# Kernel tuning notes

Hardware: AMD Instinct MI355X
Metric: run time of the kernel (lower is better)

Reference implementation:

```python
import jax, jax.numpy as jnp
import numpy as np

# Baked genome DAG structure (static per-instance in the original module)
N_IN = 256
LAYER_SIZES = [256, 256, 256, 256, 64]  # 4 hidden layers + output layer
N_OUT = LAYER_SIZES[-1]
N_EVAL = sum(LAYER_SIZES)  # 1088 eval nodes (node_evals)
DEG = 32                   # incoming links per eval node
BATCH = 8192


def setup_inputs() -> dict:
    key = jax.random.key(0)
    kx, kw, kb, kr = jax.random.split(key, 4)
    x = jax.random.normal(kx, (BATCH, N_IN), dtype=jnp.float32)
    # connection weights, node bias, node response (learned genome params)
    w = jax.random.normal(kw, (N_EVAL, DEG), dtype=jnp.float32) * 0.5
    bias = jax.random.normal(kb, (N_EVAL,), dtype=jnp.float32) * 0.1
    response = 1.0 + jax.random.normal(kr, (N_EVAL,), dtype=jnp.float32) * 0.1
    # per-layer source indices: each eval node connects to DEG earlier nodes
    src_rows = []
    offset = N_IN  # number of nodes topologically before current layer
    for li, sz in enumerate(LAYER_SIZES):
        ks = jax.random.fold_in(key, 100 + li)
        src_rows.append(jax.random.randint(ks, (sz, DEG), 0, offset, dtype=jnp.int32))
        offset += sz
    src_idx = jnp.concatenate(src_rows, axis=0)  # [N_EVAL, DEG]
    return {"x": x, "w": w, "bias": bias, "response": response, "src_idx": src_idx}


def reference(x, w, bias, response, src_idx):
    # values: [B, n_nodes_so_far]; starts as the input node values
    values = x
    row = 0
    for sz in LAYER_SIZES:  # small fixed structural loop (topological layers)
        s = src_idx[row:row + sz]                       # [sz, DEG]
        gathered = values[:, s]                         # [B, sz, DEG]
        agg = jnp.einsum('bsd,sd->bs', gathered, w[row:row + sz])  # sum aggregation
        out = jax.nn.relu(bias[row:row + sz] + response[row:row + sz] * agg)
        values = jnp.concatenate([values, out], axis=1)
        row += sz
    return values[:, -N_OUT:]  # [B, N_OUT]
```

## Files before the change

### kernel.cpp

```cpp
#include <hip/hip_runtime.h>

#define N_IN   256
#define N_EVAL 1088
#define TOTALW 1344
#define DEG    32

typedef __attribute__((ext_vector_type(8))) short short8;
typedef __attribute__((ext_vector_type(4))) float f32x4;
typedef unsigned short u16;
typedef unsigned int   u32;

__device__ __forceinline__ u32 pk2(float lo, float hi) {
    u32 ul = __float_as_uint(lo);
    u32 uh = __float_as_uint(hi);
    ul = (ul + 0x7fffu + ((ul >> 16) & 1u)) >> 16;
    uh = (uh + 0x7fffu + ((uh >> 16) & 1u)) & 0xffff0000u;
    return ul | uh;
}
__device__ __forceinline__ u16 bf1(float v) {
    u32 u = __float_as_uint(v);
    return (u16)((u + 0x7fffu + ((u >> 16) & 1u)) >> 16);
}

__global__ __launch_bounds__(256) void build_dense32(
    const int* __restrict__ src, const float* __restrict__ w,
    u32* __restrict__ B32)
{
    const int t = blockIdx.x * 256 + threadIdx.x;
    const int tile = t >> 8;
    const int q    = t & 255;
    const int lane = q >> 2;
    const int e2   = q & 3;
    int li, ts;
    if      (tile < 128)  { li = 0; ts = 0;    }
    else if (tile < 384)  { li = 1; ts = 128;  }
    else if (tile < 768)  { li = 2; ts = 384;  }
    else if (tile < 1280) { li = 3; ts = 768;  }
    else                  { li = 4; ts = 1280; }
    const int tloc = tile - ts;
    int kt, nt;
    if (li < 4) { kt = tloc >> 4; nt = tloc & 15; }
    else        { kt = tloc >> 2; nt = tloc & 3;  }
    const int ln = lane & 15, g = lane >> 4;
    const int gn = li * 256 + nt * 16 + ln;
    const int k0 = kt * 32 + g * 8 + e2 * 2;

    int c[DEG]; float ow[DEG];
    const int4*   s4 = (const int4*)(src + (size_t)gn * DEG);
    const float4* w4 = (const float4*)(w   + (size_t)gn * DEG);
    #pragma unroll
    for (int k = 0; k < 8; ++k) {
        int4 ci = s4[k]; float4 wf = w4[k];
        c[4*k+0]=ci.x; c[4*k+1]=ci.y; c[4*k+2]=ci.z; c[4*k+3]=ci.w;
        ow[4*k+0]=wf.x; ow[4*k+1]=wf.y; ow[4*k+2]=wf.z; ow[4*k+3]=wf.w;
    }
    float s0 = 0.f, s1 = 0.f;
    #pragma unroll
    for (int d = 0; d < DEG; ++d) {
        s0 += (c[d] == k0    ) ? ow[d] : 0.f;
        s1 += (c[d] == k0 + 1) ? ow[d] : 0.f;
    }
    B32[t] = pk2(s0, s1);
}

#define TILE_B 32
#define LDSCOLS 1280
#define RSTRIDE (LDSCOLS * 2)

#define MFMA(a, b, c) __builtin_amdgcn_mfma_f32_16x16x32_bf16(a, b, c, 0, 0, 0)

__global__ __launch_bounds__(512) void neat_mfma(
    const float* __restrict__ x, const u16* __restrict__ Bbuf,
    const float* __restrict__ bias, const float* __restrict__ resp,
    float* __restrict__ out)
{
    __shared__ uint4 ldsq[(TILE_B * RSTRIDE) / 16];
    __shared__ f32x4 pbuf[4 * 64 * 2];
    char* lds = (char*)ldsq;
    const int tid  = threadIdx.x;
    const int bid  = blockIdx.x;
    const int b0   = bid * TILE_B;
    const int lane = tid & 63;
    const int wvid = tid >> 6;

    const short8* Bf = (const short8*)Bbuf;
    short8 rp0[8], rp1[8];
    {
        const int rot0 = bid & 7;
        const short8* bp0 = Bf + wvid * 64 + lane;
        const short8* bp1 = Bf + (wvid + 8) * 64 + lane;
        #pragma unroll
        for (int j = 0; j < 8; ++j) {
            int ph = j + rot0; if (ph >= 8) ph -= 8;
            rp0[j] = bp0[ph * 1024];
            rp1[j] = bp1[ph * 1024];
        }
    }

    #pragma unroll
    for (int i = 0; i < 4; ++i) {
        int f4 = tid + i * 512;
        int row = f4 >> 6;
        int c4  = f4 & 63;
        float4 xv = ((const float4*)(x + (size_t)(b0 + row) * N_IN))[c4];
        u32 p0 = pk2(xv.x, xv.y), p1 = pk2(xv.z, xv.w);
        int byte = row * RSTRIDE + ((c4 * 8) ^ ((row & 7) << 4));
        *(u32*)(lds + byte)     = p0;
        *(u32*)(lds + byte + 4) = p1;
    }
    __syncthreads();

    const int r0  = lane & 15;
    const int g16 = (lane >> 4) << 4;
    const int sw  = (r0 & 7) << 4;
    const int ab0 = r0 * RSTRIDE;
    const int ab1 = (r0 + 16) * RSTRIDE;

    int cbase = N_IN;
    #pragma unroll
    for (int li = 0; li < 5; ++li) {
        const int ktn = (N_IN + li * 256) >> 5;
        const int loff8[5] = {0, 8192, 24576, 49152, 81920};
        const int lo8 = loff8[li];
        const int nbase = cbase - N_IN;

        if (li < 4) {
            const int STEP = 16 * 64;
            const int rot  = bid % ktn;
            const int nt0 = wvid, nt1 = wvid + 8;
            const short8* bp0 = Bf + lo8 + nt0 * 64 + lane;
            const short8* bp1 = Bf + lo8 + nt1 * 64 + lane;
            const int gr0 = nbase + nt0 * 16 + r0;
            const int gr1 = nbase + nt1 * 16 + r0;
            const float bb0 = bias[gr0], rr0 = resp[gr0];
            const float bb1 = bias[gr1], rr1 = resp[gr1];

            f32x4 acc00 = {0,0,0,0}, acc01 = {0,0,0,0};
            f32x4 acc10 = {0,0,0,0}, acc11 = {0,0,0,0};
            for (int kt8 = 0; kt8 < ktn; kt8 += 8) {
                #pragma unroll
                for (int j = 0; j < 8; ++j) {
                    int kt  = kt8 + j;
                    int ktp = kt + 8; if (ktp >= ktn) ktp = ktn - 1;
                    int php = ktp + rot; if (php >= ktn) php -= ktn;
                    short8 f0 = bp0[php * STEP];
                    short8 f1 = bp1[php * STEP];
                    int phk = kt + rot; if (phk >= ktn) phk -= ktn;
                    int inrow = (phk * 64 + g16) ^ sw;
                    short8 a0 = *(const short8*)(lds + ab0 + inrow);
                    short8 a1 = *(const short8*)(lds + ab1 + inrow);
                    acc00 = MFMA(a0, rp0[j], acc00);
                    acc01 = MFMA(a1, rp0[j], acc01);
                    acc10 = MFMA(a0, rp1[j], acc10);
                    acc11 = MFMA(a1, rp1[j], acc11);
                    rp0[j] = f0; rp1[j] = f1;
                }
            }

            if (li < 3) {
                const int ktnN = (N_IN + (li + 1) * 256) >> 5;
                const int rotN = bid % ktnN;
                const short8* bn0 = Bf + loff8[li + 1] + nt0 * 64 + lane;
                const short8* bn1 = Bf + loff8[li + 1] + nt1 * 64 + lane;
                #pragma unroll
                for (int j = 0; j < 8; ++j) {
                    int ph = j + rotN; if (ph >= ktnN) ph -= ktnN;
                    rp0[j] = bn0[ph * STEP];
                    rp1[j] = bn1[ph * STEP];
                }
            } else {
                const int nt4   = wvid & 3;
                const int ktbg4 = (wvid >> 2) * 20;
                const int rot4  = bid % 20;
                const short8* b4 = Bf + loff8[4] + nt4 * 64 + lane;
                #pragma unroll
                for (int j = 0; j < 4; ++j) {
                    int ph = j + rot4; if (ph >= 20) ph -= 20;
                    rp0[j] = b4[(ktbg4 + ph) * 256];
                }
            }

            #pragma unroll
            for (int t = 0; t < 2; ++t) {
                int nt = t ? nt1 : nt0;
                f32x4 aA = t ? acc10 : acc00;
                f32x4 aB = t ? acc11 : acc01;
                float bb = t ? bb1 : bb0;
                float rr = t ? rr1 : rr0;
                int colbyte = (cbase + nt * 16 + r0) * 2;
                #pragma unroll
                for (int r = 0; r < 4; ++r) {
                    int i0 = ((lane >> 4) << 2) + r;
                    float v0 = fmaxf(fmaf(rr, aA[r], bb), 0.f);
                    *(u16*)(lds + i0 * RSTRIDE + (colbyte ^ ((i0 & 7) << 4))) = bf1(v0);
                    int i1 = i0 + 16;
                    float v1 = fmaxf(fmaf(rr, aB[r], bb), 0.f);
                    *(u16*)(lds + i1 * RSTRIDE + (colbyte ^ ((i1 & 7) << 4))) = bf1(v1);
                }
            }
            __syncthreads();
        } else {
            const int STEP = 4 * 64;
            const int nt0   = wvid & 3;
            const int ktbeg = (wvid >> 2) * 20;
            const int rot4  = bid % 20;
            const short8* bp0 = Bf + lo8 + nt0 * 64 + lane;
            const int gr0 = nbase + nt0 * 16 + r0;
            const float bb0 = bias[gr0], rr0 = resp[gr0];

            f32x4 acc0 = {0,0,0,0}, acc1 = {0,0,0,0};
            for (int kt4 = 0; kt4 < 20; kt4 += 4) {
                #pragma unroll
                for (int j = 0; j < 4; ++j) {
                    int lcl  = kt4 + j;
                    int lclp = lcl + 4; if (lclp >= 20) lclp = 19;
                    int php = lclp + rot4; if (php >= 20) php -= 20;
                    short8 f0 = bp0[(ktbeg + php) * STEP];
                    int phk = lcl + rot4; if (phk >= 20) phk -= 20;
                    int inrow = ((ktbeg + phk) * 64 + g16) ^ sw;
                    short8 a0 = *(const short8*)(lds + ab0 + inrow);
                    short8 a1 = *(const short8*)(lds + ab1 + inrow);
                    acc0 = MFMA(a0, rp0[j], acc0);
                    ac1:;
                    acc1 = MFMA(a1, rp0[j], acc1);
                    rp0[j] = f0;
                }
            }
            if (wvid >= 4) {
                pbuf[((wvid - 4) * 64 + lane) * 2 + 0] = acc0;
                pbuf[((wvid - 4) * 64 + lane) * 2 + 1] = acc1;
            }
            __syncthreads();
            if (wvid < 4) {
                f32x4 q0 = pbuf[(wvid * 64 + lane) * 2 + 0];
                f32x4 q1 = pbuf[(wvid * 64 + lane) * 2 + 1];
                acc0 += q0; acc1 += q1;
                int col = nt0 * 16 + r0;
                #pragma unroll
                for (int r = 0; r < 4; ++r) {
                    int i0 = ((lane >> 4) << 2) + r;
                    out[(size_t)(b0 + i0) * 64 + col] = fmaxf(fmaf(rr0, acc0[r], bb0), 0.f);
                    int i1 = i0 + 16;
                    out[(size_t)(b0 + i1) * 64 + col] = fmaxf(fmaf(rr0, acc1[r], bb0), 0.f);
                }
            }
        }
        cbase += 256;
    }
}

#define FTILE_B 16
__device__ __forceinline__ int gbyte(int c, int h) {
    return ((c << 5) + (h << 4)) ^ (int)((((unsigned)c >> 2) & 7u) << 5);
}
__device__ __forceinline__ void fmadw(u32 d, float wv, float* acc) {
    acc[0] = fmaf(__uint_as_float(d << 16), wv, acc[0]);
    acc[1] = fmaf(__uint_as_float(d & 0xffff0000u), wv, acc[1]);
}
__device__ __forceinline__ void colacc16(const u32* vals, int c, float wv, float* acc) {
    const uint4* p = (const uint4*)((const char*)vals + gbyte(c, 0));
    uint4 a = p[0]; uint4 b = p[1];
    fmadw(a.x, wv, acc + 0);  fmadw(a.y, wv, acc + 2);
    fmadw(a.z, wv, acc + 4);  fmadw(a.w, wv, acc + 6);
    fmadw(b.x, wv, acc + 8);  fmadw(b.y, wv, acc + 10);
    fmadw(b.z, wv, acc + 12); fmadw(b.w, wv, acc + 14);
}
__global__ __launch_bounds__(256) void neat_eval_r4(
    const float* __restrict__ x, const float* __restrict__ w,
    const float* __restrict__ bias, const float* __restrict__ resp,
    const int* __restrict__ src, float* __restrict__ out)
{
    __shared__ u32 vals[TOTALW * 8];
    const int tid = threadIdx.x;
    const int b0  = blockIdx.x * FTILE_B;
    #pragma unroll
    for (int i = 0; i < 2; ++i) {
        int g = tid + i * 256;
        int c = g & 255, h = g >> 8;
        u32 pk[4];
        #pragma unroll
        for (int j = 0; j < 4; ++j) {
            float lo = x[(size_t)(b0 + h * 8 + 2 * j    ) * N_IN + c];
            float hi = x[(size_t)(b0 + h * 8 + 2 * j + 1) * N_IN + c];
            pk[j] = pk2(lo, hi);
        }
        *(uint4*)((char*)vals + gbyte(c, h)) = make_uint4(pk[0], pk[1], pk[2], pk[3]);
    }
    __syncthreads();
    int row = 0, outoff = N_IN;
    #pragma unroll
    for (int li = 0; li < 5; ++li) {
        const int sz = (li < 4) ? 256 : 64;
        for (int n = tid; n < sz; n += 256) {
            const int gr = row + n;
            const int4*   s4 = (const int4*)(src + (size_t)gr * DEG);
            const float4* w4 = (const float4*)(w   + (size_t)gr * DEG);
            float acc[16];
            #pragma unroll
            for (int i = 0; i < 16; ++i) acc[i] = 0.f;
            #pragma unroll
            for (int k = 0; k < DEG / 4; ++k) {
                int4 i4 = s4[k]; float4 wv = w4[k];
                colacc16(vals, i4.x, wv.x, acc);
                colacc16(vals, i4.y, wv.y, acc);
                colacc16(vals, i4.z, wv.z, acc);
                colacc16(vals, i4.w, wv.w, acc);
            }
            const float bb = bias[gr], rr = resp[gr];
            u32 pk[8];
            #pragma unroll
            for (int j = 0; j < 8; ++j) {
                float lo = fmaxf(fmaf(rr, acc[2 * j    ], bb), 0.f);
                float hi = fmaxf(fmaf(rr, acc[2 * j + 1], bb), 0.f);
                pk[j] = pk2(lo, hi);
            }
            int ob = gbyte(outoff + n, 0);
            *(uint4*)((char*)vals + ob)      = make_uint4(pk[0], pk[1], pk[2], pk[3]);
            *(uint4*)((char*)vals + ob + 16) = make_uint4(pk[4], pk[5], pk[6], pk[7]);
        }
        __syncthreads();
        row += sz; outoff += sz;
    }
    #pragma unroll
    for (int i = 0; i < 4; ++i) {
        int idx = tid + i * 256;
        int c = idx & 63, b = idx >> 6;
        int col = TOTALW - 64 + c;
        const u32* g = (const u32*)((const char*)vals + gbyte(col, b >> 3));
        u32 d = g[(b & 7) >> 1];
        float v = (b & 1) ? __uint_as_float(d & 0xffff0000u)
                          : __uint_as_float(d << 16);
        out[(size_t)(b0 + b) * 64 + c] = v;
    }
}

extern "C" void kernel_launch(void* const* d_in, const int* in_sizes, int n_in,
                              void* d_out, int out_size, void* d_ws, size_t ws_size,
                              hipStream_t stream) {
    const float* x    = (const float*)d_in[0];
    const float* w    = (const float*)d_in[1];
    const float* bias = (const float*)d_in[2];
    const float* resp = (const float*)d_in[3];
    const int*   src  = (const int*)d_in[4];
    float* out = (float*)d_out;

    const int batch = in_sizes[0] / N_IN;
    const size_t need = 737280ull * 2;

    if (ws_size >= need && (batch % TILE_B) == 0) {
        u32* Bbuf = (u32*)d_ws;
        build_dense32<<<1440, 256, 0, stream>>>(src, w, Bbuf);
        neat_mfma<<<batch / TILE_B, 512, 0, stream>>>(x, (const u16*)Bbuf, bias, resp, out);
    } else {
        neat_eval_r4<<<batch / FTILE_B, 256, 0, stream>>>(x, w, bias, resp, src, out);
    }
}
```

Measured before the change: 27.40 us.

## Split K dimension across two wave groups with 1024-thread blocks

Doubles the block to 16 waves and splits each hidden layer's K loop in half between two wave groups. Partial accumulators are combined through LDS before the bias/ReLU writeback, and the output layer is split four ways instead of two. The aim is more waves per block to hide latency and shorten each wave's serial MFMA chain. In exchange it adds an extra barrier and an LDS reduction per layer, and halves the register prefetch depth.

```diff
diff --git a/kernel.cpp b/kernel.cpp
--- a/kernel.cpp
+++ b/kernel.cpp
@@ -69,37 +69,39 @@
 
 #define MFMA(a, b, c) __builtin_amdgcn_mfma_f32_16x16x32_bf16(a, b, c, 0, 0, 0)
 
-__global__ __launch_bounds__(512) void neat_mfma(
+__global__ __launch_bounds__(1024, 4) void neat_mfma(
     const float* __restrict__ x, const u16* __restrict__ Bbuf,
     const float* __restrict__ bias, const float* __restrict__ resp,
     float* __restrict__ out)
 {
     __shared__ uint4 ldsq[(TILE_B * RSTRIDE) / 16];
-    __shared__ f32x4 pbuf[4 * 64 * 2];
+    __shared__ f32x4 pbuf[8 * 64 * 4];
     char* lds = (char*)ldsq;
     const int tid  = threadIdx.x;
     const int bid  = blockIdx.x;
     const int b0   = bid * TILE_B;
     const int lane = tid & 63;
     const int wvid = tid >> 6;
+    const int sub  = wvid & 7;
+    const int kw   = wvid >> 3;
 
     const short8* Bf = (const short8*)Bbuf;
-    short8 rp0[8], rp1[8];
+    short8 rp0[4], rp1[4];
     {
         const int rot0 = bid & 7;
-        const short8* bp0 = Bf + wvid * 64 + lane;
-        const short8* bp1 = Bf + (wvid + 8) * 64 + lane;
+        const short8* bp0 = Bf + sub * 64 + lane;
+        const short8* bp1 = Bf + (sub + 8) * 64 + lane;
         #pragma unroll
-        for (int j = 0; j < 8; ++j) {
-            int ph = j + rot0; if (ph >= 8) ph -= 8;
+        for (int j = 0; j < 4; ++j) {
+            int ph = kw * 4 + j + rot0; if (ph >= 8) ph -= 8;
             rp0[j] = bp0[ph * 1024];
             rp1[j] = bp1[ph * 1024];
         }
     }
 
     #pragma unroll
-    for (int i = 0; i < 4; ++i) {
-        int f4 = tid + i * 512;
+    for (int i = 0; i < 2; ++i) {
+        int f4 = tid + i * 1024;
         int row = f4 >> 6;
         int c4  = f4 & 63;
         float4 xv = ((const float4*)(x + (size_t)(b0 + row) * N_IN))[c4];
@@ -126,8 +128,10 @@
 
         if (li < 4) {
             const int STEP = 16 * 64;
+            const int kth  = ktn >> 1;
             const int rot  = bid % ktn;
-            const int nt0 = wvid, nt1 = wvid + 8;
+            const int kb   = kw * kth;
+            const int nt0 = sub, nt1 = sub + 8;
             const short8* bp0 = Bf + lo8 + nt0 * 64 + lane;
             const short8* bp1 = Bf + lo8 + nt1 * 64 + lane;
             const int gr0 = nbase + nt0 * 16 + r0;
@@ -137,15 +141,15 @@
 
             f32x4 acc00 = {0,0,0,0}, acc01 = {0,0,0,0};
             f32x4 acc10 = {0,0,0,0}, acc11 = {0,0,0,0};
-            for (int kt8 = 0; kt8 < ktn; kt8 += 8) {
-                #pragma unroll
-                for (int j = 0; j < 8; ++j) {
-                    int kt  = kt8 + j;
-                    int ktp = kt + 8; if (ktp >= ktn) ktp = ktn - 1;
-                    int php = ktp + rot; if (php >= ktn) php -= ktn;
+            for (int lcl4 = 0; lcl4 < kth; lcl4 += 4) {
+                #pragma unroll
+                for (int j = 0; j < 4; ++j) {
+                    int lcl  = lcl4 + j;
+                    int lclp = lcl + 4; if (lclp >= kth) lclp = kth - 1;
+                    int php = kb + lclp + rot; if (php >= ktn) php -= ktn;
                     short8 f0 = bp0[php * STEP];
                     short8 f1 = bp1[php * STEP];
-                    int phk = kt + rot; if (phk >= ktn) phk -= ktn;
+                    int phk = kb + lcl + rot; if (phk >= ktn) phk -= ktn;
                     int inrow = (phk * 64 + g16) ^ sw;
                     short8 a0 = *(const short8*)(lds + ab0 + inrow);
                     short8 a1 = *(const short8*)(lds + ab1 + inrow);
@@ -159,83 +163,95 @@
 
             if (li < 3) {
                 const int ktnN = (N_IN + (li + 1) * 256) >> 5;
+                const int kthN = ktnN >> 1;
                 const int rotN = bid % ktnN;
                 const short8* bn0 = Bf + loff8[li + 1] + nt0 * 64 + lane;
                 const short8* bn1 = Bf + loff8[li + 1] + nt1 * 64 + lane;
                 #pragma unroll
-                for (int j = 0; j < 8; ++j) {
-                    int ph = j + rotN; if (ph >= ktnN) ph -= ktnN;
+                for (int j = 0; j < 4; ++j) {
+                    int ph = kw * kthN + j + rotN; if (ph >= ktnN) ph -= ktnN;
                     rp0[j] = bn0[ph * STEP];
                     rp1[j] = bn1[ph * STEP];
                 }
             } else {
-                const int nt4   = wvid & 3;
-                const int ktbg4 = (wvid >> 2) * 20;
-                const int rot4  = bid % 20;
+                const int nt4 = wvid & 3;
+                const int ks4 = wvid >> 2;
+                const int rot4 = bid % 40;
                 const short8* b4 = Bf + loff8[4] + nt4 * 64 + lane;
                 #pragma unroll
                 for (int j = 0; j < 4; ++j) {
-                    int ph = j + rot4; if (ph >= 20) ph -= 20;
-                    rp0[j] = b4[(ktbg4 + ph) * 256];
-                }
-            }
-
-            #pragma unroll
-            for (int t = 0; t < 2; ++t) {
-                int nt = t ? nt1 : nt0;
-                f32x4 aA = t ? acc10 : acc00;
-                f32x4 aB = t ? acc11 : acc01;
-                float bb = t ? bb1 : bb0;
-                float rr = t ? rr1 : rr0;
-                int colbyte = (cbase + nt * 16 + r0) * 2;
-                #pragma unroll
-                for (int r = 0; r < 4; ++r) {
-                    int i0 = ((lane >> 4) << 2) + r;
-                    float v0 = fmaxf(fmaf(rr, aA[r], bb), 0.f);
-                    *(u16*)(lds + i0 * RSTRIDE + (colbyte ^ ((i0 & 7) << 4))) = bf1(v0);
-                    int i1 = i0 + 16;
-                    float v1 = fmaxf(fmaf(rr, aB[r], bb), 0.f);
-                    *(u16*)(lds + i1 * RSTRIDE + (colbyte ^ ((i1 & 7) << 4))) = bf1(v1);
+                    int ph = ks4 * 10 + j + rot4; if (ph >= 40) ph -= 40;
+                    rp0[j] = b4[ph * 256];
+                }
+            }
+
+            if (kw == 1) {
+                int pb = (sub * 64 + lane) * 4;
+                pbuf[pb + 0] = acc00; pbuf[pb + 1] = acc01;
+                pbuf[pb + 2] = acc10; pbuf[pb + 3] = acc11;
+            }
+            __syncthreads();
+            if (kw == 0) {
+                int pb = (sub * 64 + lane) * 4;
+                acc00 += pbuf[pb + 0]; acc01 += pbuf[pb + 1];
+                acc10 += pbuf[pb + 2]; acc11 += pbuf[pb + 3];
+                #pragma unroll
+                for (int t = 0; t < 2; ++t) {
+                    int nt = t ? nt1 : nt0;
+                    f32x4 aA = t ? acc10 : acc00;
+                    f32x4 aB = t ? acc11 : acc01;
+                    float bb = t ? bb1 : bb0;
+                    float rr = t ? rr1 : rr0;
+                    int colbyte = (cbase + nt * 16 + r0) * 2;
+                    #pragma unroll
+                    for (int r = 0; r < 4; ++r) {
+                        int i0 = ((lane >> 4) << 2) + r;
+                        float v0 = fmaxf(fmaf(rr, aA[r], bb), 0.f);
+                        *(u16*)(lds + i0 * RSTRIDE + (colbyte ^ ((i0 & 7) << 4))) = bf1(v0);
+                        int i1 = i0 + 16;
+                        float v1 = fmaxf(fmaf(rr, aB[r], bb), 0.f);
+                        *(u16*)(lds + i1 * RSTRIDE + (colbyte ^ ((i1 & 7) << 4))) = bf1(v1);
+                    }
                 }
             }
             __syncthreads();
         } else {
             const int STEP = 4 * 64;
-            const int nt0   = wvid & 3;
-            const int ktbeg = (wvid >> 2) * 20;
-            const int rot4  = bid % 20;
-            const short8* bp0 = Bf + lo8 + nt0 * 64 + lane;
-            const int gr0 = nbase + nt0 * 16 + r0;
+            const int nt4  = wvid & 3;
+            const int kseg = wvid >> 2;
+            const int rot4 = bid % 40;
+            const short8* bp0 = Bf + lo8 + nt4 * 64 + lane;
+            const int gr0 = nbase + nt4 * 16 + r0;
             const float bb0 = bias[gr0], rr0 = resp[gr0];
 
             f32x4 acc0 = {0,0,0,0}, acc1 = {0,0,0,0};
-            for (int kt4 = 0; kt4 < 20; kt4 += 4) {
-                #pragma unroll
-                for (int j = 0; j < 4; ++j) {
-                    int lcl  = kt4 + j;
-                    int lclp = lcl + 4; if (lclp >= 20) lclp = 19;
-                    int php = lclp + rot4; if (php >= 20) php -= 20;
-                    short8 f0 = bp0[(ktbeg + php) * STEP];
-                    int phk = lcl + rot4; if (phk >= 20) phk -= 20;
-                    int inrow = ((ktbeg + phk) * 64 + g16) ^ sw;
-                    short8 a0 = *(const short8*)(lds + ab0 + inrow);
-                    short8 a1 = *(const short8*)(lds + ab1 + inrow);
-                    acc0 = MFMA(a0, rp0[j], acc0);
-                    ac1:;
-                    acc1 = MFMA(a1, rp0[j], acc1);
-                    rp0[j] = f0;
-                }
-            }
-            if (wvid >= 4) {
-                pbuf[((wvid - 4) * 64 + lane) * 2 + 0] = acc0;
-                pbuf[((wvid - 4) * 64 + lane) * 2 + 1] = acc1;
+            #pragma unroll
+            for (int lcl = 0; lcl < 10; ++lcl) {
+                int lclp = lcl + 4; if (lclp >= 10) lclp = 9;
+                int php = kseg * 10 + lclp + rot4; if (php >= 40) php -= 40;
+                short8 f0 = bp0[php * STEP];
+                int phk = kseg * 10 + lcl + rot4; if (phk >= 40) phk -= 40;
+                int inrow = (phk * 64 + g16) ^ sw;
+                short8 a0 = *(const short8*)(lds + ab0 + inrow);
+                short8 a1 = *(const short8*)(lds + ab1 + inrow);
+                acc0 = MFMA(a0, rp0[lcl & 3], acc0);
+                acc1 = MFMA(a1, rp0[lcl & 3], acc1);
+                rp0[lcl & 3] = f0;
+            }
+            if (kseg >= 1) {
+                int pb = (((kseg - 1) * 4 + nt4) * 64 + lane) * 2;
+                pbuf[pb + 0] = acc0;
+                pbuf[pb + 1] = acc1;
             }
             __syncthreads();
-            if (wvid < 4) {
-                f32x4 q0 = pbuf[(wvid * 64 + lane) * 2 + 0];
-                f32x4 q1 = pbuf[(wvid * 64 + lane) * 2 + 1];
-                acc0 += q0; acc1 += q1;
-                int col = nt0 * 16 + r0;
+            if (kseg == 0) {
+                #pragma unroll
+                for (int s = 0; s < 3; ++s) {
+                    int pb = ((s * 4 + nt4) * 64 + lane) * 2;
+                    acc0 += pbuf[pb + 0];
+                    acc1 += pbuf[pb + 1];
+                }
+                int col = nt4 * 16 + r0;
                 #pragma unroll
                 for (int r = 0; r < 4; ++r) {
                     int i0 = ((lane >> 4) << 2) + r;
@@ -350,7 +366,7 @@
     if (ws_size >= need && (batch % TILE_B) == 0) {
         u32* Bbuf = (u32*)d_ws;
         build_dense32<<<1440, 256, 0, stream>>>(src, w, Bbuf);
-        neat_mfma<<<batch / TILE_B, 512, 0, stream>>>(x, (const u16*)Bbuf, bias, resp, out);
+        neat_mfma<<<batch / TILE_B, 1024, 0, stream>>>(x, (const u16*)Bbuf, bias, resp, out);
     } else {
         neat_eval_r4<<<batch / FTILE_B, 256, 0, stream>>>(x, w, bias, resp, src, out);
     }
```

New measurement: 29.30 us. 1.07x slower.

## Double batch tile to 64 rows per block and drop split-K in output layer

Applied to the files above, without the earlier changes.

Raises the batch tile from 32 to 64 rows, so each wave issues eight MFMAs per B fragment instead of four, halving global weight traffic per row. The output layer now runs on four waves over the full 40 k-steps, which removes the LDS partial-sum buffer and its extra barrier. In exchange, LDS use roughly doubles to about 160KB per block and only half as many blocks are launched. This can leave many CUs idle and serialises the final layer on half the waves.

```diff
diff --git a/kernel.cpp b/kernel.cpp
--- a/kernel.cpp
+++ b/kernel.cpp
@@ -63,19 +63,18 @@
     B32[t] = pk2(s0, s1);
 }
 
-#define TILE_B 32
+#define TILE_B 64
 #define LDSCOLS 1280
 #define RSTRIDE (LDSCOLS * 2)
 
 #define MFMA(a, b, c) __builtin_amdgcn_mfma_f32_16x16x32_bf16(a, b, c, 0, 0, 0)
 
-__global__ __launch_bounds__(512) void neat_mfma(
+__global__ __launch_bounds__(512, 2) void neat_mfma(
     const float* __restrict__ x, const u16* __restrict__ Bbuf,
     const float* __restrict__ bias, const float* __restrict__ resp,
     float* __restrict__ out)
 {
     __shared__ uint4 ldsq[(TILE_B * RSTRIDE) / 16];
-    __shared__ f32x4 pbuf[4 * 64 * 2];
     char* lds = (char*)ldsq;
     const int tid  = threadIdx.x;
     const int bid  = blockIdx.x;
@@ -98,7 +97,7 @@
     }
 
     #pragma unroll
-    for (int i = 0; i < 4; ++i) {
+    for (int i = 0; i < 8; ++i) {
         int f4 = tid + i * 512;
         int row = f4 >> 6;
         int c4  = f4 & 63;
@@ -115,6 +114,8 @@
     const int sw  = (r0 & 7) << 4;
     const int ab0 = r0 * RSTRIDE;
     const int ab1 = (r0 + 16) * RSTRIDE;
+    const int ab2 = (r0 + 32) * RSTRIDE;
+    const int ab3 = (r0 + 48) * RSTRIDE;
 
     int cbase = N_IN;
     #pragma unroll
@@ -135,8 +136,10 @@
             const float bb0 = bias[gr0], rr0 = resp[gr0];
             const float bb1 = bias[gr1], rr1 = resp[gr1];
 
-            f32x4 acc00 = {0,0,0,0}, acc01 = {0,0,0,0};
-            f32x4 acc10 = {0,0,0,0}, acc11 = {0,0,0,0};
+            f32x4 ac0[4], ac1[4];
+            #pragma unroll
+            for (int m = 0; m < 4; ++m) { ac0[m] = (f32x4){0,0,0,0}; ac1[m] = (f32x4){0,0,0,0}; }
+
             for (int kt8 = 0; kt8 < ktn; kt8 += 8) {
                 #pragma unroll
                 for (int j = 0; j < 8; ++j) {
@@ -149,10 +152,16 @@
                     int inrow = (phk * 64 + g16) ^ sw;
                     short8 a0 = *(const short8*)(lds + ab0 + inrow);
                     short8 a1 = *(const short8*)(lds + ab1 + inrow);
-                    acc00 = MFMA(a0, rp0[j], acc00);
-                    acc01 = MFMA(a1, rp0[j], acc01);
-                    acc10 = MFMA(a0, rp1[j], acc10);
-                    acc11 = MFMA(a1, rp1[j], acc11);
+                    short8 a2 = *(const short8*)(lds + ab2 + inrow);
+                    short8 a3 = *(const short8*)(lds + ab3 + inrow);
+                    ac0[0] = MFMA(a0, rp0[j], ac0[0]);
+                    ac0[1] = MFMA(a1, rp0[j], ac0[1]);
+                    ac0[2] = MFMA(a2, rp0[j], ac0[2]);
+                    ac0[3] = MFMA(a3, rp0[j], ac0[3]);
+                    ac1[0] = MFMA(a0, rp1[j], ac1[0]);
+                    ac1[1] = MFMA(a1, rp1[j], ac1[1]);
+                    ac1[2] = MFMA(a2, rp1[j], ac1[2]);
+                    ac1[3] = MFMA(a3, rp1[j], ac1[3]);
                     rp0[j] = f0; rp1[j] = f1;
                 }
             }
@@ -168,80 +177,75 @@
                     rp0[j] = bn0[ph * STEP];
                     rp1[j] = bn1[ph * STEP];
                 }
-            } else {
-                const int nt4   = wvid & 3;
-                const int ktbg4 = (wvid >> 2) * 20;
-                const int rot4  = bid % 20;
-                const short8* b4 = Bf + loff8[4] + nt4 * 64 + lane;
-                #pragma unroll
-                for (int j = 0; j < 4; ++j) {
-                    int ph = j + rot4; if (ph >= 20) ph -= 20;
-                    rp0[j] = b4[(ktbg4 + ph) * 256];
+            } else if (wvid < 4) {
+                const int rot4 = bid % 40;
+                const short8* b4 = Bf + loff8[4] + wvid * 64 + lane;
+                #pragma unroll
+                for (int j = 0; j < 8; ++j) {
+                    int ph = j + rot4; if (ph >= 40) ph -= 40;
+                    rp0[j] = b4[ph * 256];
                 }
             }
 
             #pragma unroll
             for (int t = 0; t < 2; ++t) {
                 int nt = t ? nt1 : nt0;
-                f32x4 aA = t ? acc10 : acc00;
-                f32x4 aB = t ? acc11 : acc01;
                 float bb = t ? bb1 : bb0;
                 float rr = t ? rr1 : rr0;
                 int colbyte = (cbase + nt * 16 + r0) * 2;
                 #pragma unroll
-                for (int r = 0; r < 4; ++r) {
-                    int i0 = ((lane >> 4) << 2) + r;
-                    float v0 = fmaxf(fmaf(rr, aA[r], bb), 0.f);
-                    *(u16*)(lds + i0 * RSTRIDE + (colbyte ^ ((i0 & 7) << 4))) = bf1(v0);
-                    int i1 = i0 + 16;
-                    float v1 = fmaxf(fmaf(rr, aB[r], bb), 0.f);
-                    *(u16*)(lds + i1 * RSTRIDE + (colbyte ^ ((i1 & 7) << 4))) = bf1(v1);
+                for (int m = 0; m < 4; ++m) {
+                    f32x4 aA = t ? ac1[m] : ac0[m];
+                    #pragma unroll
+                    for (int r = 0; r < 4; ++r) {
+                        int i0 = m * 16 + ((lane >> 4) << 2) + r;
+                        float v0 = fmaxf(fmaf(rr, aA[r], bb), 0.f);
+                        *(u16*)(lds + i0 * RSTRIDE + (colbyte ^ ((i0 & 7) << 4))) = bf1(v0);
+                    }
                 }
             }
             __syncthreads();
         } else {
-            const int STEP = 4 * 64;
-            const int nt0   = wvid & 3;
-            const int ktbeg = (wvid >> 2) * 20;
-            const int rot4  = bid % 20;
-            const short8* bp0 = Bf + lo8 + nt0 * 64 + lane;
-            const int gr0 = nbase + nt0 * 16 + r0;
-            const float bb0 = bias[gr0], rr0 = resp[gr0];
-
-            f32x4 acc0 = {0,0,0,0}, acc1 = {0,0,0,0};
-            for (int kt4 = 0; kt4 < 20; kt4 += 4) {
-                #pragma unroll
-                for (int j = 0; j < 4; ++j) {
-                    int lcl  = kt4 + j;
-                    int lclp = lcl + 4; if (lclp >= 20) lclp = 19;
-                    int php = lclp + rot4; if (php >= 20) php -= 20;
-                    short8 f0 = bp0[(ktbeg + php) * STEP];
-                    int phk = lcl + rot4; if (phk >= 20) phk -= 20;
-                    int inrow = ((ktbeg + phk) * 64 + g16) ^ sw;
-                    short8 a0 = *(const short8*)(lds + ab0 + inrow);
-                    short8 a1 = *(const short8*)(lds + ab1 + inrow);
-                    acc0 = MFMA(a0, rp0[j], acc0);
-                    ac1:;
-                    acc1 = MFMA(a1, rp0[j], acc1);
-                    rp0[j] = f0;
-                }
-            }
-            if (wvid >= 4) {
-                pbuf[((wvid - 4) * 64 + lane) * 2 + 0] = acc0;
-                pbuf[((wvid - 4) * 64 + lane) * 2 + 1] = acc1;
-            }
-            __syncthreads();
             if (wvid < 4) {
-                f32x4 q0 = pbuf[(wvid * 64 + lane) * 2 + 0];
-                f32x4 q1 = pbuf[(wvid * 64 + lane) * 2 + 1];
-                acc0 += q0; acc1 += q1;
-                int col = nt0 * 16 + r0;
-                #pragma unroll
-                for (int r = 0; r < 4; ++r) {
-                    int i0 = ((lane >> 4) << 2) + r;
-                    out[(size_t)(b0 + i0) * 64 + col] = fmaxf(fmaf(rr0, acc0[r], bb0), 0.f);
-                    int i1 = i0 + 16;
-                    out[(size_t)(b0 + i1) * 64 + col] = fmaxf(fmaf(rr0, acc1[r], bb0), 0.f);
+                const int STEP = 4 * 64;
+                const int nt4  = wvid;
+                const int rot4 = bid % 40;
+                const short8* bp0 = Bf + lo8 + nt4 * 64 + lane;
+                const int gr0 = nbase + nt4 * 16 + r0;
+                const float bb0 = bias[gr0], rr0 = resp[gr0];
+
+                f32x4 ac[4];
+                #pragma unroll
+                for (int m = 0; m < 4; ++m) ac[m] = (f32x4){0,0,0,0};
+
+                for (int kt8 = 0; kt8 < 40; kt8 += 8) {
+                    #pragma unroll
+                    for (int j = 0; j < 8; ++j) {
+                        int kt  = kt8 + j;
+                        int ktp = kt + 8; if (ktp >= 40) ktp = 39;
+                        int php = ktp + rot4; if (php >= 40) php -= 40;
+                        short8 f0 = bp0[php * STEP];
+                        int phk = kt + rot4; if (phk >= 40) phk -= 40;
+                        int inrow = (phk * 64 + g16) ^ sw;
+                        short8 a0 = *(const short8*)(lds + ab0 + inrow);
+                        short8 a1 = *(const short8*)(lds + ab1 + inrow);
+                        short8 a2 = *(const short8*)(lds + ab2 + inrow);
+                        short8 a3 = *(const short8*)(lds + ab3 + inrow);
+                        ac[0] = MFMA(a0, rp0[j], ac[0]);
+                        ac[1] = MFMA(a1, rp0[j], ac[1]);
+                        ac[2] = MFMA(a2, rp0[j], ac[2]);
+                        ac[3] = MFMA(a3, rp0[j], ac[3]);
+                        rp0[j] = f0;
+                    }
+                }
+                int col = nt4 * 16 + r0;
+                #pragma unroll
+                for (int m = 0; m < 4; ++m) {
+                    #pragma unroll
+                    for (int r = 0; r < 4; ++r) {
+                        int i0 = m * 16 + ((lane >> 4) << 2) + r;
+                        out[(size_t)(b0 + i0) * 64 + col] = fmaxf(fmaf(rr0, ac[m][r], bb0), 0.f);
+                    }
                 }
             }
         }
```

After: 34.94 us. 1.28x slower.
